# Performance work log

Hardware: AMD Instinct MI355X
Metric: run time of the kernel (lower is better)

## Reference

```python
import jax, jax.numpy as jnp
import numpy as np

B, S, H, NH = 2, 2048, 1024, 16
HD = H // NH  # 64


def setup_inputs() -> dict:
    key = jax.random.key(0)
    ks = jax.random.split(key, 9)
    s = 1.0 / np.sqrt(H)
    d = {"x": jax.random.normal(ks[0], (B, S, H), jnp.float32)}
    for i, n in enumerate(["Wq", "Wk", "Wv", "Wo"]):
        d[n] = jax.random.normal(ks[1 + i], (H, H), jnp.float32) * s
    for i, n in enumerate(["bq", "bk", "bv", "bo"]):
        d[n] = jax.random.normal(ks[5 + i], (H,), jnp.float32) * s
    return d


def _heads(x, W, b):
    # torch nn.Linear: y = x @ W.T + b, then split heads -> (B, NH, S, HD)
    y = x @ W.T + b
    return y.reshape(B, S, NH, HD).transpose(0, 2, 1, 3)


def _tetra_channels(t):
    # tetrapoint vector [a, 1-a, a*(1-a), clamp(1-(a+(1-a)),0,1)] for a scalar slice t
    a = jax.nn.sigmoid(t)
    na = 1.0 - a
    neither = jnp.clip(1.0 - (a + na), 0.0, 1.0)
    return jnp.stack([a, na, a * na, neither], axis=-1)  # (..., 4)


def reference(x, Wq, bq, Wk, bk, Wv, bv, Wo, bo):
    Q = _heads(x, Wq, bq)  # (B, NH, S, HD)
    K = _heads(x, Wk, bk)
    V = _heads(x, Wv, bv)
    # Original indexes Q_tetrapoints[:, :, :, 0] on [B,NH,S,HD,4]: selects head-dim
    # slot 0 (resp. 2) and keeps the 4 tetrapoint channels -> (B, NH, S, 4).
    Qa = _tetra_channels(Q[..., 0])
    Ka = _tetra_channels(K[..., 0])
    Qb = _tetra_channels(Q[..., 2])
    Kb = _tetra_channels(K[..., 2])
    scores = (jnp.einsum('bhsc,bhtc->bhst', Qa, Ka) / np.sqrt(HD)
              + 0.1 * jnp.einsum('bhsc,bhtc->bhst', Qb, Kb))  # (B, NH, S, S)
    w = jax.nn.softmax(scores, axis=-1)
    out = jnp.einsum('bhst,bhtd->bhsd', w, V)  # (B, NH, S, HD)
    out = out.transpose(0, 2, 1, 3).reshape(B, S, H)
    return out @ Wo.T + bo
```

## Files before the change

kernel.cpp:

```cpp
#include <hip/hip_runtime.h>
#include <hip/hip_bf16.h>

#define SS 2048
#define HH 1024
#define NHH 16
#define HDD 64

using f32x4  = __attribute__((ext_vector_type(4))) float;
using bf16x8 = __attribute__((ext_vector_type(8))) short;

#if __has_builtin(__builtin_amdgcn_exp2f)
#define EXP2F __builtin_amdgcn_exp2f
#else
#define EXP2F exp2f
#endif

__device__ __forceinline__ unsigned short f2bf(float f) {
    unsigned u = __builtin_bit_cast(unsigned, f);
    unsigned r = u + 0x7FFFu + ((u >> 16) & 1u);
    return (unsigned short)(r >> 16);
}

__device__ __forceinline__ unsigned bfround(float f) {
    unsigned u = __builtin_bit_cast(unsigned, f);
    return u + 0x7FFFu + ((u >> 16) & 1u);
}
__device__ __forceinline__ unsigned pack2bf(float a, float b) {
    return __builtin_amdgcn_perm(bfround(b), bfround(a), 0x07060302u);
}
__device__ __forceinline__ unsigned pack2bf_trunc(float a, float b) {
    return __builtin_amdgcn_perm(__builtin_bit_cast(unsigned, b),
                                 __builtin_bit_cast(unsigned, a), 0x07060302u);
}

__device__ __forceinline__ void tetra(float t, float* c) {
    float a = 1.f / (1.f + __expf(-t));
    float na = 1.f - a;
    float nei = 1.f - (a + na);
    nei = fminf(fmaxf(nei, 0.f), 1.f);
    c[0] = a; c[1] = na; c[2] = a * na; c[3] = nei;
}

__device__ __forceinline__ void gll16(const unsigned short* g, unsigned short* l) {
    __builtin_amdgcn_global_load_lds(
        (const __attribute__((address_space(1))) unsigned int*)g,
        (__attribute__((address_space(3))) unsigned int*)l, 16, 0, 0);
}

__global__ __launch_bounds__(256) void cvt_kernel(
    const float* __restrict__ x, const float* __restrict__ Wv, const float* __restrict__ Wo,
    const float* __restrict__ Wq, const float* __restrict__ Wk,
    const float* __restrict__ bq, const float* __restrict__ bk,
    unsigned short* __restrict__ xb, unsigned short* __restrict__ Wvb, unsigned short* __restrict__ Wob,
    unsigned short* __restrict__ wselb, float* __restrict__ bselws)
{
    if (blockIdx.x >= 2048) {
        int n = blockIdx.x - 2048;
        int h = n >> 2, q = n & 3;
        int rowIdx = h * HDD + ((q & 1) ? 2 : 0);
        const float* src  = (q & 2) ? Wk : Wq;
        const float* bsrc = (q & 2) ? bk : bq;
        int t = threadIdx.x;
        float4 v = *(const float4*)(src + (size_t)rowIdx * HH + t * 4);
        uint2 pk;
        pk.x = pack2bf(v.x, v.y);
        pk.y = pack2bf(v.z, v.w);
        *(uint2*)(wselb + (size_t)n * HH + t * 4) = pk;
        if (t == 0) bselws[n] = bsrc[rowIdx];
        return;
    }
    size_t gid = (size_t)blockIdx.x * 256 + threadIdx.x;
    size_t base = gid * 8;
    {
        float4 a = *(const float4*)(x + base);
        float4 b = *(const float4*)(x + base + 4);
        uint4 pk;
        pk.x = pack2bf(a.x, a.y);
        pk.y = pack2bf(a.z, a.w);
        pk.z = pack2bf(b.x, b.y);
        pk.w = pack2bf(b.z, b.w);
        *(uint4*)(xb + base) = pk;
    }
    if (base < 1048576) {
        float4 a = *(const float4*)(Wv + base);
        float4 b = *(const float4*)(Wv + base + 4);
        uint4 pk;
        pk.x = pack2bf(a.x, a.y);
        pk.y = pack2bf(a.z, a.w);
        pk.z = pack2bf(b.x, b.y);
        pk.w = pack2bf(b.z, b.w);
        *(uint4*)(Wvb + base) = pk;
        a = *(const float4*)(Wo + base);
        b = *(const float4*)(Wo + base + 4);
        pk.x = pack2bf(a.x, a.y);
        pk.y = pack2bf(a.z, a.w);
        pk.z = pack2bf(b.x, b.y);
        pk.w = pack2bf(b.z, b.w);
        *(uint4*)(Wob + base) = pk;
    }
}

template<int OUT_MODE>
__device__ __forceinline__ void gemm_body(unsigned char* smem,
    const unsigned short* __restrict__ A, const unsigned short* __restrict__ Bw,
    const float* __restrict__ bias, void* __restrict__ Cout, int bx, int by)
{
    int tid = threadIdx.x;
    int wave = tid >> 6, lane = tid & 63;
    int l15 = lane & 15, l16 = lane >> 4;
    int wm = wave >> 1, wn = wave & 1;
    int m0 = by * 128, n0 = bx * 64;

    int lrow = lane >> 3;
    int lcolsw = ((lane & 7) ^ lrow) * 8;
    const unsigned short* Ag = A + (size_t)(m0 + wave * 32 + lrow) * HH + lcolsw;
    const unsigned short* Bg = Bw + (size_t)(n0 + wave * 16 + lrow) * HH + lcolsw;

    f32x4 acc[4][2] = {};

    {
        unsigned short* As = (unsigned short*)smem + (size_t)wave * 32 * 64;
        unsigned short* Bs = (unsigned short*)(smem + 16384) + (size_t)wave * 16 * 64;
        #pragma unroll
        for (int i = 0; i < 4; i++)
            gll16(Ag + (size_t)(i * 8) * HH, As + i * 8 * 64);
        #pragma unroll
        for (int i = 0; i < 2; i++)
            gll16(Bg + (size_t)(i * 8) * HH, Bs + i * 8 * 64);
    }
    __syncthreads();

    int swq = l15 & 7;
    int cur = 0;
    for (int k0 = 0; k0 < HH; k0 += 64) {
        if (k0 + 64 < HH) {
            unsigned char* nb = smem + (cur ^ 1) * 24576;
            unsigned short* As = (unsigned short*)nb + (size_t)wave * 32 * 64;
            unsigned short* Bs = (unsigned short*)(nb + 16384) + (size_t)wave * 16 * 64;
            #pragma unroll
            for (int i = 0; i < 4; i++)
                gll16(Ag + (size_t)(i * 8) * HH + k0 + 64, As + i * 8 * 64);
            #pragma unroll
            for (int i = 0; i < 2; i++)
                gll16(Bg + (size_t)(i * 8) * HH + k0 + 64, Bs + i * 8 * 64);
        }

        unsigned char* cb = smem + cur * 24576;
        #pragma unroll
        for (int kk = 0; kk < 2; kk++) {
            int csw = ((kk * 4 + l16) ^ swq) * 16;
            bf16x8 af[4], bfr[2];
            #pragma unroll
            for (int mi = 0; mi < 4; mi++)
                af[mi] = *(const bf16x8*)(cb + (wm * 64 + mi * 16 + l15) * 128 + csw);
            #pragma unroll
            for (int ni = 0; ni < 2; ni++)
                bfr[ni] = *(const bf16x8*)(cb + 16384 + (wn * 32 + ni * 16 + l15) * 128 + csw);
            #pragma unroll
            for (int mi = 0; mi < 4; mi++)
                #pragma unroll
                for (int ni = 0; ni < 2; ni++)
                    acc[mi][ni] = __builtin_amdgcn_mfma_f32_16x16x32_bf16(af[mi], bfr[ni], acc[mi][ni], 0, 0, 0);
        }
        __syncthreads();
        cur ^= 1;
    }

    float bv[2];
    #pragma unroll
    for (int ni = 0; ni < 2; ni++)
        bv[ni] = bias[n0 + wn * 32 + ni * 16 + l15];

    #pragma unroll
    for (int mi = 0; mi < 4; mi++) {
        #pragma unroll
        for (int ni = 0; ni < 2; ni++) {
            int n = n0 + wn * 32 + ni * 16 + l15;
            if (OUT_MODE == 0) {
                #pragma unroll
                for (int r = 0; r < 4; r++) {
                    int m = m0 + wm * 64 + mi * 16 + l16 * 4 + r;
                    ((float*)Cout)[(size_t)m * HH + n] = acc[mi][ni][r] + bv[ni];
                }
            } else {
                int m = m0 + wm * 64 + mi * 16 + l16 * 4;
                int b = m >> 11, s = m & 2047;
                int h = n >> 6, d = n & 63;
                uint2 pk;
                pk.x = pack2bf(acc[mi][ni][0] + bv[ni], acc[mi][ni][1] + bv[ni]);
                pk.y = pack2bf(acc[mi][ni][2] + bv[ni], acc[mi][ni][3] + bv[ni]);
                *(uint2*)((unsigned short*)Cout + ((size_t)((b * NHH + h) * HDD + d)) * SS + s) = pk;
            }
        }
    }
}

__device__ __forceinline__ void qk_body(unsigned char* smem,
    const unsigned short* __restrict__ xb, const unsigned short* __restrict__ wselb,
    const float* __restrict__ bselws,
    unsigned short* __restrict__ qfb, unsigned short* __restrict__ kfb, int blk)
{
    auto xs = (unsigned short (*)[72])smem;
    auto ws = (unsigned short (*)[72])(smem + 4608);
    auto ys = (float (*)[68])(smem + 13824);
    int tid = threadIdx.x;
    int wave = tid >> 6, lane = tid & 63;
    int l15 = lane & 15, l16 = lane >> 4;
    int m0 = blk * 32;
    int n0w = wave * 16;

    int xr = tid >> 3, xseg = (tid & 7) * 8;
    int wr = tid >> 2, wseg = (tid & 3) * 16;
    const unsigned short* xp = xb + (size_t)(m0 + xr) * HH + xseg;
    const unsigned short* wp = wselb + (size_t)wr * HH + wseg;

    f32x4 acc[2] = {};

    uint4 xv  = *(const uint4*)(xp);
    uint4 wv0 = *(const uint4*)(wp);
    uint4 wv1 = *(const uint4*)(wp + 8);

    for (int k0 = 0; k0 < HH; k0 += 64) {
        __syncthreads();
        *(uint4*)&xs[xr][xseg] = xv;
        *(uint4*)&ws[wr][wseg]     = wv0;
        *(uint4*)&ws[wr][wseg + 8] = wv1;
        __syncthreads();

        int kn = (k0 + 64) & (HH - 1);
        uint4 nxv  = *(const uint4*)(xp + kn);
        uint4 nwv0 = *(const uint4*)(wp + kn);
        uint4 nwv1 = *(const uint4*)(wp + kn + 8);

        #pragma unroll
        for (int kk = 0; kk < 64; kk += 32) {
            bf16x8 bfr = *(const bf16x8*)&ws[n0w + l15][kk + l16 * 8];
            #pragma unroll
            for (int mi = 0; mi < 2; mi++) {
                bf16x8 af = *(const bf16x8*)&xs[mi * 16 + l15][kk + l16 * 8];
                acc[mi] = __builtin_amdgcn_mfma_f32_16x16x32_bf16(af, bfr, acc[mi], 0, 0, 0);
            }
        }
        xv = nxv; wv0 = nwv0; wv1 = nwv1;
    }

    float bias = bselws[n0w + l15];
    __syncthreads();
    #pragma unroll
    for (int mi = 0; mi < 2; mi++)
        #pragma unroll
        for (int r = 0; r < 4; r++)
            ys[mi * 16 + l16 * 4 + r][n0w + l15] = acc[mi][r] + bias;
    __syncthreads();

    #pragma unroll
    for (int pass = 0; pass < 2; pass++) {
        int ml = tid & 31;
        int h = (tid >> 5) + pass * 8;
        float4 y4 = *(const float4*)&ys[ml][h * 4];
        float qa[4], qb2[4], ka[4], kb2[4];
        tetra(y4.x, qa);
        tetra(y4.y, qb2);
        tetra(y4.z, ka);
        tetra(y4.w, kb2);
        int m = m0 + ml, b = m >> 11, s = m & 2047;
        size_t base = ((size_t)(b * NHH + h) * SS + s) * 8;
        const float sA = 0.18033688011112042f;
        const float sB = 0.14426950408889634f;
        uint4 qp, kp;
        qp.x = pack2bf(qa[0] * sA, qa[1] * sA);
        qp.y = pack2bf(qa[2] * sA, qa[3] * sA);
        qp.z = pack2bf(qb2[0] * sB, qb2[1] * sB);
        qp.w = pack2bf(qb2[2] * sB, qb2[3] * sB);
        kp.x = pack2bf(ka[0], ka[1]);
        kp.y = pack2bf(ka[2], ka[3]);
        kp.z = pack2bf(kb2[0], kb2[1]);
        kp.w = pack2bf(kb2[2], kb2[3]);
        *(uint4*)(qfb + base) = qp;
        *(uint4*)(kfb + base) = kp;
    }
}

__global__ __launch_bounds__(256) void fused_mid(
    const unsigned short* __restrict__ xb,
    const unsigned short* __restrict__ Wvb, const float* __restrict__ bv,
    unsigned short* __restrict__ Vt,
    const unsigned short* __restrict__ wselb, const float* __restrict__ bselws,
    unsigned short* __restrict__ qfb, unsigned short* __restrict__ kfb)
{
    __shared__ __align__(16) unsigned char smem[49152];
    int p = blockIdx.x;
    if (p < 512) {
        int id = (p & 7) * 64 + (p >> 3);
        gemm_body<2>(smem, xb, Wvb, bv, Vt, id & 15, id >> 4);
    } else {
        int q = p - 512;
        int id = (q & 7) * 16 + (q >> 3);
        qk_body(smem, xb, wselb, bselws, qfb, kfb, id);
    }
}

__global__ __launch_bounds__(256) void gemm_out(
    const unsigned short* __restrict__ A, const unsigned short* __restrict__ Bw,
    const float* __restrict__ bias, float* __restrict__ Cout)
{
    __shared__ __align__(16) unsigned char smem[49152];
    int p = blockIdx.x;
    int id = (p & 7) * 64 + (p >> 3);
    gemm_body<0>(smem, A, Bw, bias, Cout, id & 15, id >> 4);
}

__global__ __launch_bounds__(512) void attn_mfma(
    const unsigned short* __restrict__ qfb, const unsigned short* __restrict__ kfb,
    const unsigned short* __restrict__ Vt, unsigned short* __restrict__ attnb)
{
    __shared__ __align__(16) unsigned char lds[65536];

    int tid = threadIdx.x;
    int wave = tid >> 6, lane = tid & 63;
    int sub = wave & 3, hf = wave >> 2;
    int l15 = lane & 15, l16 = lane >> 4;
    int l7 = l15 & 7;

    int L = blockIdx.x + (blockIdx.y << 4);
    int logical = ((L & 7) << 6) + (L >> 3);
    int bh = logical >> 4, qblk = logical & 15;
    int b = bh >> 4, h = bh & 15;
    int s0 = qblk * 128 + sub * 32;

    bf16x8 qA = {0,0,0,0,0,0,0,0}, qB = {0,0,0,0,0,0,0,0};
    if (l16 == 0) {
        qA = *(const bf16x8*)(qfb + ((size_t)bh * SS + s0 + l15) * 8);
        qB = *(const bf16x8*)(qfb + ((size_t)bh * SS + s0 + 16 + l15) * 8);
    }

    const short oneb = 0x3F80;
    bf16x8 ones = {oneb,oneb,oneb,oneb,oneb,oneb,oneb,oneb};

    const unsigned short* kfA = kfb + ((size_t)bh * SS + hf * 1024 + l15) * 8;

    int t8 = tid & 255, shf = tid >> 8;
    int vd = t8 >> 2, vr = t8 & 3;
    const unsigned short* vsrc = Vt + ((size_t)bh * HDD + vd) * SS + shf * 1024 + vr * 16;

    unsigned char* vrow = lds + shf * 16384 + vd * 128;
    int sw0 = ((vr * 2)     ^ (vd & 7)) << 4;
    int sw1 = ((vr * 2 + 1) ^ (vd & 7)) << 4;
    unsigned char* psw = lds + 32768 + wave * 4096;

    f32x4 acc[2][4] = {};
    f32x4 accl[2] = {};

    {
        uint4 t0a = *(const uint4*)(vsrc);
        uint4 t0b = *(const uint4*)(vsrc + 8);
        *(uint4*)(vrow + sw0) = t0a;
        *(uint4*)(vrow + sw1) = t0b;
    }
    uint4 sv0 = *(const uint4*)(vsrc + 64);
    uint4 sv1 = *(const uint4*)(vsrc + 64 + 8);
    bf16x8 kfr[4];
    #pragma unroll
    for (int tb = 0; tb < 4; tb++)
        kfr[tb] = *(const bf16x8*)(kfA + (size_t)(tb * 16) * 8);

    for (int it = 0; it < 16; it++) {
        __syncthreads();

        int nb = (it + 1) & 1;
        *(uint4*)(vrow + nb * 8192 + sw0) = sv0;
        *(uint4*)(vrow + nb * 8192 + sw1) = sv1;

        int tv = ((it + 2) & 15) << 6;
        uint4 nv0 = *(const uint4*)(vsrc + tv);
        uint4 nv1 = *(const uint4*)(vsrc + tv + 8);
        int tkf = ((it + 1) & 15) << 6;
        bf16x8 nkf[4];
        #pragma unroll
        for (int tb = 0; tb < 4; tb++)
            nkf[tb] = *(const bf16x8*)(kfA + (size_t)(tkf + tb * 16) * 8);

        #pragma unroll
        for (int g = 0; g < 2; g++) {
            bf16x8 qf = g ? qB : qA;
            #pragma unroll
            for (int tb = 0; tb < 4; tb++) {
                f32x4 sc = {};
                sc = __builtin_amdgcn_mfma_f32_16x16x32_bf16(kfr[tb], qf, sc, 0, 0, 0);
                uint2 pw;
                pw.x = pack2bf_trunc(EXP2F(sc[0]), EXP2F(sc[1]));
                pw.y = pack2bf_trunc(EXP2F(sc[2]), EXP2F(sc[3]));
                int qr = g * 16 + l15;
                int c  = (tb * 2 + (l16 >> 1)) ^ l7;
                *(uint2*)(psw + qr * 128 + c * 16 + (l16 & 1) * 8) = pw;
            }
        }

        unsigned char* vbuf = lds + hf * 16384 + (it & 1) * 8192;
        __builtin_amdgcn_s_setprio(1);
        #pragma unroll
        for (int tk = 0; tk < 2; tk++) {
            int csw = ((tk * 4 + l16) ^ l7) << 4;
            bf16x8 apA = *(const bf16x8*)(psw + l15 * 128 + csw);
            bf16x8 apB = *(const bf16x8*)(psw + (16 + l15) * 128 + csw);
            accl[0] = __builtin_amdgcn_mfma_f32_16x16x32_bf16(apA, ones, accl[0], 0, 0, 0);
            accl[1] = __builtin_amdgcn_mfma_f32_16x16x32_bf16(apB, ones, accl[1], 0, 0, 0);
            #pragma unroll
            for (int nd = 0; nd < 4; nd++) {
                bf16x8 bv = *(const bf16x8*)(vbuf + (nd * 16 + l15) * 128 + csw);
                acc[0][nd] = __builtin_amdgcn_mfma_f32_16x16x32_bf16(apA, bv, acc[0][nd], 0, 0, 0);
                acc[1][nd] = __builtin_amdgcn_mfma_f32_16x16x32_bf16(apB, bv, acc[1][nd], 0, 0, 0);
            }
        }
        __builtin_amdgcn_s_setprio(0);

        sv0 = nv0; sv1 = nv1;
        #pragma unroll
        for (int tb = 0; tb < 4; tb++) kfr[tb] = nkf[tb];
    }

    __syncthreads();
    float* xch = (float*)lds;
    if (wave >= 4) {
        float* dst = xch + ((size_t)((wave - 4) * 64 + lane)) * 40;
        #pragma unroll
        for (int g = 0; g < 2; g++)
            #pragma unroll
            for (int nd = 0; nd < 4; nd++)
                *(f32x4*)(dst + (g * 4 + nd) * 4) = acc[g][nd];
        *(f32x4*)(dst + 32) = accl[0];
        *(f32x4*)(dst + 36) = accl[1];
    }
    __syncthreads();
    if (wave < 4) {
        float* src = xch + ((size_t)(wave * 64 + lane)) * 40;
        #pragma unroll
        for (int g = 0; g < 2; g++)
            #pragma unroll
            for (int nd = 0; nd < 4; nd++)
                acc[g][nd] += *(const f32x4*)(src + (g * 4 + nd) * 4);
        accl[0] += *(const f32x4*)(src + 32);
        accl[1] += *(const f32x4*)(src + 36);

        #pragma unroll
        for (int g = 0; g < 2; g++) {
            #pragma unroll
            for (int r = 0; r < 4; r++) {
                float linv = 1.f / accl[g][r];
                int q = s0 + g * 16 + l16 * 4 + r;
                size_t row = (size_t)(b * SS + q) * HH + h * HDD;
                #pragma unroll
                for (int nd = 0; nd < 4; nd++)
                    attnb[row + nd * 16 + l15] = f2bf(acc[g][nd][r] * linv);
            }
        }
    }
}

extern "C" void kernel_launch(void* const* d_in, const int* in_sizes, int n_in,
                              void* d_out, int out_size, void* d_ws, size_t ws_size,
                              hipStream_t stream)
{
    const float* x  = (const float*)d_in[0];
    const float* Wq = (const float*)d_in[1];
    const float* Wk = (const float*)d_in[2];
    const float* Wv = (const float*)d_in[3];
    const float* Wo = (const float*)d_in[4];
    const float* bq = (const float*)d_in[5];
    const float* bk = (const float*)d_in[6];
    const float* bv = (const float*)d_in[7];
    const float* bo = (const float*)d_in[8];

    unsigned short* qfb   = (unsigned short*)d_ws;
    unsigned short* kfb   = qfb + 524288;
    unsigned short* xb    = kfb + 524288;
    unsigned short* attnb = xb;
    unsigned short* Wvb   = xb + 4194304;
    unsigned short* Wob   = Wvb + 1048576;
    unsigned short* Vt    = Wob + 1048576;
    unsigned short* wselb  = Vt + 4194304;
    float*          bselws = (float*)(wselb + 65536);

    cvt_kernel<<<2112, 256, 0, stream>>>(x, Wv, Wo, Wq, Wk, bq, bk, xb, Wvb, Wob, wselb, bselws);
    fused_mid<<<640, 256, 0, stream>>>(xb, Wvb, bv, Vt, wselb, bselws, qfb, kfb);
    attn_mfma<<<dim3(16, 32), 512, 0, stream>>>(qfb, kfb, Vt, attnb);
    gemm_out<<<512, 256, 0, stream>>>(attnb, Wob, bo, (float*)d_out);
}
```

Measured before the change: 149.5 us.

## Enlarge GEMM tiles to 128x128 with 512-thread blocks

The shared GEMM body used by the V projection and the output projection now computes 128x128 output tiles with eight waves instead of 128x64 with four. The LDS double buffer grows to 64 KB, and the launch grids are halved to 256 GEMM blocks. The intent is more operand reuse per block and less repeated global and LDS traffic for A. The QK-feature body shares the same 512-thread kernel, so its upper four waves redo the same work and write identical results. Occupancy per CU drops and a single block wave must cover all CUs.

```diff
diff --git a/kernel.cpp b/kernel.cpp
--- a/kernel.cpp
+++ b/kernel.cpp
@@ -109,24 +109,23 @@
     int wave = tid >> 6, lane = tid & 63;
     int l15 = lane & 15, l16 = lane >> 4;
     int wm = wave >> 1, wn = wave & 1;
-    int m0 = by * 128, n0 = bx * 64;
+    int m0 = by * 128, n0 = bx * 128;
 
     int lrow = lane >> 3;
     int lcolsw = ((lane & 7) ^ lrow) * 8;
-    const unsigned short* Ag = A + (size_t)(m0 + wave * 32 + lrow) * HH + lcolsw;
+    const unsigned short* Ag = A + (size_t)(m0 + wave * 16 + lrow) * HH + lcolsw;
     const unsigned short* Bg = Bw + (size_t)(n0 + wave * 16 + lrow) * HH + lcolsw;
 
-    f32x4 acc[4][2] = {};
+    f32x4 acc[2][4] = {};
 
     {
-        unsigned short* As = (unsigned short*)smem + (size_t)wave * 32 * 64;
-        unsigned short* Bs = (unsigned short*)(smem + 16384) + (size_t)wave * 16 * 64;
-        #pragma unroll
-        for (int i = 0; i < 4; i++)
+        unsigned short* As = (unsigned short*)smem + (size_t)(wave * 16) * 64;
+        unsigned short* Bs = (unsigned short*)(smem + 16384) + (size_t)(wave * 16) * 64;
+        #pragma unroll
+        for (int i = 0; i < 2; i++) {
             gll16(Ag + (size_t)(i * 8) * HH, As + i * 8 * 64);
-        #pragma unroll
-        for (int i = 0; i < 2; i++)
             gll16(Bg + (size_t)(i * 8) * HH, Bs + i * 8 * 64);
+        }
     }
     __syncthreads();
 
@@ -134,56 +133,55 @@
     int cur = 0;
     for (int k0 = 0; k0 < HH; k0 += 64) {
         if (k0 + 64 < HH) {
-            unsigned char* nb = smem + (cur ^ 1) * 24576;
-            unsigned short* As = (unsigned short*)nb + (size_t)wave * 32 * 64;
-            unsigned short* Bs = (unsigned short*)(nb + 16384) + (size_t)wave * 16 * 64;
-            #pragma unroll
-            for (int i = 0; i < 4; i++)
+            unsigned char* nb = smem + (cur ^ 1) * 32768;
+            unsigned short* As = (unsigned short*)nb + (size_t)(wave * 16) * 64;
+            unsigned short* Bs = (unsigned short*)(nb + 16384) + (size_t)(wave * 16) * 64;
+            #pragma unroll
+            for (int i = 0; i < 2; i++) {
                 gll16(Ag + (size_t)(i * 8) * HH + k0 + 64, As + i * 8 * 64);
-            #pragma unroll
-            for (int i = 0; i < 2; i++)
                 gll16(Bg + (size_t)(i * 8) * HH + k0 + 64, Bs + i * 8 * 64);
-        }
-
-        unsigned char* cb = smem + cur * 24576;
+            }
+        }
+
+        unsigned char* cb = smem + cur * 32768;
         #pragma unroll
         for (int kk = 0; kk < 2; kk++) {
             int csw = ((kk * 4 + l16) ^ swq) * 16;
-            bf16x8 af[4], bfr[2];
-            #pragma unroll
-            for (int mi = 0; mi < 4; mi++)
-                af[mi] = *(const bf16x8*)(cb + (wm * 64 + mi * 16 + l15) * 128 + csw);
-            #pragma unroll
-            for (int ni = 0; ni < 2; ni++)
-                bfr[ni] = *(const bf16x8*)(cb + 16384 + (wn * 32 + ni * 16 + l15) * 128 + csw);
-            #pragma unroll
-            for (int mi = 0; mi < 4; mi++)
+            bf16x8 af[2], bfr[4];
+            #pragma unroll
+            for (int mi = 0; mi < 2; mi++)
+                af[mi] = *(const bf16x8*)(cb + (wm * 32 + mi * 16 + l15) * 128 + csw);
+            #pragma unroll
+            for (int ni = 0; ni < 4; ni++)
+                bfr[ni] = *(const bf16x8*)(cb + 16384 + (wn * 64 + ni * 16 + l15) * 128 + csw);
+            #pragma unroll
+            for (int mi = 0; mi < 2; mi++)
                 #pragma unroll
-                for (int ni = 0; ni < 2; ni++)
+                for (int ni = 0; ni < 4; ni++)
                     acc[mi][ni] = __builtin_amdgcn_mfma_f32_16x16x32_bf16(af[mi], bfr[ni], acc[mi][ni], 0, 0, 0);
         }
         __syncthreads();
         cur ^= 1;
     }
 
-    float bv[2];
+    float bv[4];
     #pragma unroll
-    for (int ni = 0; ni < 2; ni++)
-        bv[ni] = bias[n0 + wn * 32 + ni * 16 + l15];
+    for (int ni = 0; ni < 4; ni++)
+        bv[ni] = bias[n0 + wn * 64 + ni * 16 + l15];
 
     #pragma unroll
-    for (int mi = 0; mi < 4; mi++) {
-        #pragma unroll
-        for (int ni = 0; ni < 2; ni++) {
-            int n = n0 + wn * 32 + ni * 16 + l15;
+    for (int mi = 0; mi < 2; mi++) {
+        #pragma unroll
+        for (int ni = 0; ni < 4; ni++) {
+            int n = n0 + wn * 64 + ni * 16 + l15;
             if (OUT_MODE == 0) {
                 #pragma unroll
                 for (int r = 0; r < 4; r++) {
-                    int m = m0 + wm * 64 + mi * 16 + l16 * 4 + r;
+                    int m = m0 + wm * 32 + mi * 16 + l16 * 4 + r;
                     ((float*)Cout)[(size_t)m * HH + n] = acc[mi][ni][r] + bv[ni];
                 }
             } else {
-                int m = m0 + wm * 64 + mi * 16 + l16 * 4;
+                int m = m0 + wm * 32 + mi * 16 + l16 * 4;
                 int b = m >> 11, s = m & 2047;
                 int h = n >> 6, d = n & 63;
                 uint2 pk;
@@ -204,13 +202,14 @@
     auto ws = (unsigned short (*)[72])(smem + 4608);
     auto ys = (float (*)[68])(smem + 13824);
     int tid = threadIdx.x;
-    int wave = tid >> 6, lane = tid & 63;
+    int t8 = tid & 255;
+    int wave4 = (tid >> 6) & 3, lane = tid & 63;
     int l15 = lane & 15, l16 = lane >> 4;
     int m0 = blk * 32;
-    int n0w = wave * 16;
-
-    int xr = tid >> 3, xseg = (tid & 7) * 8;
-    int wr = tid >> 2, wseg = (tid & 3) * 16;
+    int n0w = wave4 * 16;
+
+    int xr = t8 >> 3, xseg = (t8 & 7) * 8;
+    int wr = t8 >> 2, wseg = (t8 & 3) * 16;
     const unsigned short* xp = xb + (size_t)(m0 + xr) * HH + xseg;
     const unsigned short* wp = wselb + (size_t)wr * HH + wseg;
 
@@ -255,8 +254,8 @@
 
     #pragma unroll
     for (int pass = 0; pass < 2; pass++) {
-        int ml = tid & 31;
-        int h = (tid >> 5) + pass * 8;
+        int ml = t8 & 31;
+        int h = (t8 >> 5) + pass * 8;
         float4 y4 = *(const float4*)&ys[ml][h * 4];
         float qa[4], qb2[4], ka[4], kb2[4];
         tetra(y4.x, qa);
@@ -281,33 +280,33 @@
     }
 }
 
-__global__ __launch_bounds__(256) void fused_mid(
+__global__ __launch_bounds__(512) void fused_mid(
     const unsigned short* __restrict__ xb,
     const unsigned short* __restrict__ Wvb, const float* __restrict__ bv,
     unsigned short* __restrict__ Vt,
     const unsigned short* __restrict__ wselb, const float* __restrict__ bselws,
     unsigned short* __restrict__ qfb, unsigned short* __restrict__ kfb)
 {
-    __shared__ __align__(16) unsigned char smem[49152];
+    __shared__ __align__(16) unsigned char smem[65536];
     int p = blockIdx.x;
-    if (p < 512) {
-        int id = (p & 7) * 64 + (p >> 3);
-        gemm_body<2>(smem, xb, Wvb, bv, Vt, id & 15, id >> 4);
+    if (p < 256) {
+        int id = (p & 7) * 32 + (p >> 3);
+        gemm_body<2>(smem, xb, Wvb, bv, Vt, id & 7, id >> 3);
     } else {
-        int q = p - 512;
+        int q = p - 256;
         int id = (q & 7) * 16 + (q >> 3);
         qk_body(smem, xb, wselb, bselws, qfb, kfb, id);
     }
 }
 
-__global__ __launch_bounds__(256) void gemm_out(
+__global__ __launch_bounds__(512) void gemm_out(
     const unsigned short* __restrict__ A, const unsigned short* __restrict__ Bw,
     const float* __restrict__ bias, float* __restrict__ Cout)
 {
-    __shared__ __align__(16) unsigned char smem[49152];
+    __shared__ __align__(16) unsigned char smem[65536];
     int p = blockIdx.x;
-    int id = (p & 7) * 64 + (p >> 3);
-    gemm_body<0>(smem, A, Bw, bias, Cout, id & 15, id >> 4);
+    int id = (p & 7) * 32 + (p >> 3);
+    gemm_body<0>(smem, A, Bw, bias, Cout, id & 7, id >> 3);
 }
 
 __global__ __launch_bounds__(512) void attn_mfma(
@@ -482,7 +481,7 @@
     float*          bselws = (float*)(wselb + 65536);
 
     cvt_kernel<<<2112, 256, 0, stream>>>(x, Wv, Wo, Wq, Wk, bq, bk, xb, Wvb, Wob, wselb, bselws);
-    fused_mid<<<640, 256, 0, stream>>>(xb, Wvb, bv, Vt, wselb, bselws, qfb, kfb);
+    fused_mid<<<384, 512, 0, stream>>>(xb, Wvb, bv, Vt, wselb, bselws, qfb, kfb);
     attn_mfma<<<dim3(16, 32), 512, 0, stream>>>(qfb, kfb, Vt, attnb);
-    gemm_out<<<512, 256, 0, stream>>>(attnb, Wob, bo, (float*)d_out);
-}
+    gemm_out<<<256, 512, 0, stream>>>(attnb, Wob, bo, (float*)d_out);
+}
```

New measurement: 152.9 us. +2.3%, slower.
